# Kernel tuning notes

Measured on AMD Instinct MI355X. Metric: run time of the kernel, lower is better.

Reference implementation:

```python
import jax, jax.numpy as jnp
import numpy as np

N = 131072   # number of profile points
S = 64       # n_samples (PSF samples per point)
D = H = W = 256


def setup_inputs() -> dict:
    key = jax.random.key(0)
    k1, k2, k3, k4, k5, k6 = jax.random.split(key, 6)
    x = jax.random.normal(k1, (1, 1, D, H, W), dtype=jnp.float32)
    # voxel-space coordinates (x, y, z) inside the volume
    sampleGrid = jax.random.uniform(k2, (N, 3), dtype=jnp.float32) * jnp.array(
        [W - 1, H - 1, D - 1], dtype=jnp.float32)
    # small axis-angle rotations + translations: [N, 1, 6]
    rot = jax.random.normal(k3, (N, 1, 3), dtype=jnp.float32) * 0.02
    trn = jax.random.normal(k4, (N, 1, 3), dtype=jnp.float32) * 2.0
    ax = jnp.concatenate([rot, trn], axis=-1)
    half = jax.random.uniform(k5, (N, 1, 3), minval=1.0, maxval=3.0, dtype=jnp.float32)
    bound = jnp.concatenate([-half, half], axis=1)  # [N, 2, 3]
    InvCovScaled = jnp.eye(3, dtype=jnp.float32) * 0.5
    # torch.randn(...) - 0.5 from the original forward, hoisted out for determinism
    xyz_psf = jax.random.normal(k6, (N, S, 3), dtype=jnp.float32) - 0.5
    return dict(x=x, sampleGrid=sampleGrid, ax=ax, bound=bound,
                InvCovScaled=InvCovScaled, xyz_psf=xyz_psf)


def _axisangle2mat(a):
    # a: [N, 6] -> [N, 3, 4] = [R | t] via Rodrigues
    v, t = a[:, :3], a[:, 3:]
    theta = jnp.linalg.norm(v, axis=-1, keepdims=True)          # [N,1]
    k = v / jnp.maximum(theta, 1e-12)                            # unit axis
    kx, ky, kz = k[:, 0], k[:, 1], k[:, 2]
    z = jnp.zeros_like(kx)
    K = jnp.stack([z, -kz, ky, kz, z, -kx, -ky, kx, z], axis=-1).reshape(-1, 3, 3)
    ct = jnp.cos(theta)[..., None]  # [N,1,1]
    st = jnp.sin(theta)[..., None]
    I = jnp.eye(3, dtype=a.dtype)
    R = I + st * K + (1.0 - ct) * jnp.matmul(K, K)
    return jnp.concatenate([R, t[..., None]], axis=-1)           # [N,3,4]


def _grid_sample_3d(vol, grid):
    # vol: [D,H,W]; grid: [M,3] normalized coords (x,y,z) in [-1,1]
    # matches F.grid_sample(mode='bilinear', padding_mode='zeros', align_corners=False)
    d, h, w = vol.shape
    sizes = jnp.array([w, h, d], dtype=vol.dtype)
    pix = ((grid + 1.0) * sizes - 1.0) * 0.5                     # unnormalize
    ix, iy, iz = pix[:, 0], pix[:, 1], pix[:, 2]
    x0 = jnp.floor(ix); y0 = jnp.floor(iy); z0 = jnp.floor(iz)
    fx = ix - x0; fy = iy - y0; fz = iz - z0
    x0 = x0.astype(jnp.int32); y0 = y0.astype(jnp.int32); z0 = z0.astype(jnp.int32)

    def gather(xi, yi, zi):
        valid = ((xi >= 0) & (xi < w) & (yi >= 0) & (yi < h) & (zi >= 0) & (zi < d))
        xc = jnp.clip(xi, 0, w - 1)
        yc = jnp.clip(yi, 0, h - 1)
        zc = jnp.clip(zi, 0, d - 1)
        return jnp.where(valid, vol[zc, yc, xc], jnp.zeros((), vol.dtype))

    out = jnp.zeros(grid.shape[0], dtype=vol.dtype)
    for dx in (0, 1):
        wx = fx if dx else (1.0 - fx)
        for dy in (0, 1):
            wy = fy if dy else (1.0 - fy)
            for dz in (0, 1):
                wz = fz if dz else (1.0 - fz)
                out = out + gather(x0 + dx, y0 + dy, z0 + dz) * (wx * wy * wz)
    return out


def reference(x, sampleGrid, ax, bound, InvCovScaled, xyz_psf):
    vol = x[0, 0]                                                # [D,H,W]
    size = jnp.array([x.shape[-1], x.shape[-2], x.shape[-3]], dtype=x.dtype)  # [W,H,D]

    # pose matrices [N,1,3,4]
    mat = _axisangle2mat(ax.reshape(-1, 6)).reshape(ax.shape[:-1] + (3, 4))
    R = mat[..., :3]                                             # [N,1,3,3]
    T = mat[..., 3]                                              # [N,1,3]
    # trans_first=True: p' = R @ (p + T)
    p = sampleGrid[:, None] + T                                  # [N,1,3]
    mat_sampleGrid = jnp.einsum('nkij,nkj->nki', R, p)           # [N,1,3]

    # PSF offsets: [N,S,3]
    bound_psf = xyz_psf * ((bound[:, 1, :] - bound[:, 0, :]) * 0.5)[:, None]
    psf = mat_sampleGrid + bound_psf                             # [N,S,3]

    grid = 2.0 * (psf / (size - 1.0) - 0.5)                      # normalize per-axis
    psf_x = _grid_sample_3d(vol, grid.reshape(-1, 3)).reshape(psf.shape[:-1])  # [N,S]

    center = bound_psf
    q = jnp.einsum('nsi,ij,nsj->ns', center, InvCovScaled, center)
    w = jnp.exp(-0.5 * q)                                        # [N,S]
    y = (psf_x * w).sum(-1) / w.sum(-1)                          # [N]
    return y
```

## Files before the change

### kernel.cpp

```cpp
#include <hip/hip_runtime.h>


#define VOL_N 256
#define S_PSF 64
#define NBUCKET 4096


__device__ __forceinline__ int bucket_of(const float* __restrict__ sg, int n) {
    int cx = min(max((int)sg[n * 3 + 0], 0), VOL_N - 1) >> 4;
    int cy = min(max((int)sg[n * 3 + 1], 0), VOL_N - 1) >> 4;
    int cz = min(max((int)sg[n * 3 + 2], 0), VOL_N - 1) >> 4;
    int m = 0;
    #pragma unroll
    for (int b = 0; b < 4; b++) {
        m |= (((cx >> b) & 1) << (3 * b))
           | (((cy >> b) & 1) << (3 * b + 1))
           | (((cz >> b) & 1) << (3 * b + 2));
    }
    return m;
}

__global__ void zero_hist_kernel(int* __restrict__ ws) {
    int i = blockIdx.x * blockDim.x + threadIdx.x;
    if (i < NBUCKET) ws[i] = 0;
}

__global__ void hist_kernel(const float* __restrict__ sg, int* __restrict__ ws, int N) {
    int n = blockIdx.x * blockDim.x + threadIdx.x;
    if (n >= N) return;
    atomicAdd(&ws[bucket_of(sg, n)], 1);
}

__global__ __launch_bounds__(1024) void scan_kernel(int* __restrict__ ws) {
    __shared__ int tmp[1024];
    const int t = threadIdx.x;
    int h0 = ws[t * 4 + 0], h1 = ws[t * 4 + 1], h2 = ws[t * 4 + 2], h3 = ws[t * 4 + 3];
    int s = h0 + h1 + h2 + h3;
    tmp[t] = s;
    __syncthreads();
    for (int off = 1; off < 1024; off <<= 1) {
        int v = (t >= off) ? tmp[t - off] : 0;
        __syncthreads();
        tmp[t] += v;
        __syncthreads();
    }
    int excl = tmp[t] - s;
    ws[NBUCKET + t * 4 + 0] = excl;
    ws[NBUCKET + t * 4 + 1] = excl + h0;
    ws[NBUCKET + t * 4 + 2] = excl + h0 + h1;
    ws[NBUCKET + t * 4 + 3] = excl + h0 + h1 + h2;
}

__global__ void scatter_kernel(const float* __restrict__ sg, int* __restrict__ ws, int N) {
    int n = blockIdx.x * blockDim.x + threadIdx.x;
    if (n >= N) return;
    int b = bucket_of(sg, n);
    int pos = atomicAdd(&ws[NBUCKET + b], 1);
    ws[2 * NBUCKET + pos] = n;
}

__global__ __launch_bounds__(256, 4) void psf_sample_kernel(
    const float* __restrict__ vol,
    const float* __restrict__ sampleGrid,
    const float* __restrict__ ax,
    const float* __restrict__ bound,
    const float* __restrict__ invcov,
    const float* __restrict__ xyz_psf,
    const int* __restrict__ perm,
    float* __restrict__ out,
    int N)
{
    const int lane = threadIdx.x & 63;

    int bid = blockIdx.x;
    const int nb = gridDim.x;
    if ((nb & 7) == 0) bid = (bid & 7) * (nb >> 3) + (bid >> 3);

    const int i = bid * (blockDim.x >> 6) + (threadIdx.x >> 6);
    if (i >= N) return;
    const int n = perm ? perm[i] : i;

    const float vx = ax[n * 6 + 0], vy = ax[n * 6 + 1], vz = ax[n * 6 + 2];
    const float tx = ax[n * 6 + 3], ty = ax[n * 6 + 4], tz = ax[n * 6 + 5];

    const float theta = sqrtf(vx * vx + vy * vy + vz * vz);
    const float kinv = 1.0f / fmaxf(theta, 1e-12f);
    const float kx = vx * kinv, ky = vy * kinv, kz = vz * kinv;
    const float ct = __cosf(theta), st = __sinf(theta);
    const float oc = 1.0f - ct;

    const float r00 = 1.0f + oc * (-(ky * ky + kz * kz));
    const float r01 = -st * kz + oc * kx * ky;
    const float r02 =  st * ky + oc * kx * kz;
    const float r10 =  st * kz + oc * kx * ky;
    const float r11 = 1.0f + oc * (-(kx * kx + kz * kz));
    const float r12 = -st * kx + oc * ky * kz;
    const float r20 = -st * ky + oc * kx * kz;
    const float r21 =  st * kx + oc * ky * kz;
    const float r22 = 1.0f + oc * (-(kx * kx + ky * ky));

    const float px = sampleGrid[n * 3 + 0] + tx;
    const float py = sampleGrid[n * 3 + 1] + ty;
    const float pz = sampleGrid[n * 3 + 2] + tz;

    const float cx = r00 * px + r01 * py + r02 * pz;
    const float cy = r10 * px + r11 * py + r12 * pz;
    const float cz = r20 * px + r21 * py + r22 * pz;

    const float hx = (bound[n * 6 + 3] - bound[n * 6 + 0]) * 0.5f;
    const float hy = (bound[n * 6 + 4] - bound[n * 6 + 1]) * 0.5f;
    const float hz = (bound[n * 6 + 5] - bound[n * 6 + 2]) * 0.5f;

    const float m00 = invcov[0], m01 = invcov[1], m02 = invcov[2];
    const float m10 = invcov[3], m11 = invcov[4], m12 = invcov[5];
    const float m20 = invcov[6], m21 = invcov[7], m22 = invcov[8];

    const long long base = ((long long)n * S_PSF + lane) * 3;
    const float ox = xyz_psf[base + 0] * hx;
    const float oy = xyz_psf[base + 1] * hy;
    const float oz = xyz_psf[base + 2] * hz;

    const float scale = (float)VOL_N / (float)(VOL_N - 1);
    const float ix = (cx + ox) * scale - 0.5f;
    const float iy = (cy + oy) * scale - 0.5f;
    const float iz = (cz + oz) * scale - 0.5f;

    const float x0f = floorf(ix), y0f = floorf(iy), z0f = floorf(iz);
    const float fx = ix - x0f, fy = iy - y0f, fz = iz - z0f;
    const int x0 = (int)x0f, y0 = (int)y0f, z0 = (int)z0f;
    const int x1 = x0 + 1, y1 = y0 + 1, z1 = z0 + 1;

    const bool vx0 = (unsigned)x0 < (unsigned)VOL_N;
    const bool vx1 = (unsigned)x1 < (unsigned)VOL_N;
    const bool vy0 = (unsigned)y0 < (unsigned)VOL_N;
    const bool vy1 = (unsigned)y1 < (unsigned)VOL_N;
    const bool vz0 = (unsigned)z0 < (unsigned)VOL_N;
    const bool vz1 = (unsigned)z1 < (unsigned)VOL_N;

    const int xc0 = min(max(x0, 0), VOL_N - 1);
    const int xc1 = min(max(x1, 0), VOL_N - 1);
    const int yc0 = min(max(y0, 0), VOL_N - 1);
    const int yc1 = min(max(y1, 0), VOL_N - 1);
    const int zc0 = min(max(z0, 0), VOL_N - 1);
    const int zc1 = min(max(z1, 0), VOL_N - 1);

    const int zo0 = zc0 * (VOL_N * VOL_N), zo1 = zc1 * (VOL_N * VOL_N);
    const int yo0 = yc0 * VOL_N, yo1 = yc1 * VOL_N;

    const float v000 = vol[zo0 + yo0 + xc0];
    const float v001 = vol[zo0 + yo0 + xc1];
    const float v010 = vol[zo0 + yo1 + xc0];
    const float v011 = vol[zo0 + yo1 + xc1];
    const float v100 = vol[zo1 + yo0 + xc0];
    const float v101 = vol[zo1 + yo0 + xc1];
    const float v110 = vol[zo1 + yo1 + xc0];
    const float v111 = vol[zo1 + yo1 + xc1];

    const float wx0 = 1.0f - fx, wx1 = fx;
    const float wy0 = 1.0f - fy, wy1 = fy;
    const float wz0 = 1.0f - fz, wz1 = fz;

    float acc = 0.0f;
    acc += (vx0 && vy0 && vz0) ? v000 * (wx0 * wy0 * wz0) : 0.0f;
    acc += (vx1 && vy0 && vz0) ? v001 * (wx1 * wy0 * wz0) : 0.0f;
    acc += (vx0 && vy1 && vz0) ? v010 * (wx0 * wy1 * wz0) : 0.0f;
    acc += (vx1 && vy1 && vz0) ? v011 * (wx1 * wy1 * wz0) : 0.0f;
    acc += (vx0 && vy0 && vz1) ? v100 * (wx0 * wy0 * wz1) : 0.0f;
    acc += (vx1 && vy0 && vz1) ? v101 * (wx1 * wy0 * wz1) : 0.0f;
    acc += (vx0 && vy1 && vz1) ? v110 * (wx0 * wy1 * wz1) : 0.0f;
    acc += (vx1 && vy1 && vz1) ? v111 * (wx1 * wy1 * wz1) : 0.0f;

    const float qx = m00 * ox + m01 * oy + m02 * oz;
    const float qy = m10 * ox + m11 * oy + m12 * oz;
    const float qz = m20 * ox + m21 * oy + m22 * oz;
    const float q = ox * qx + oy * qy + oz * qz;
    const float w = __expf(-0.5f * q);

    float num = acc * w;
    float den = w;
    #pragma unroll
    for (int m = 32; m >= 1; m >>= 1) {
        num += __shfl_xor(num, m, 64);
        den += __shfl_xor(den, m, 64);
    }
    if (lane == 0) out[n] = num / den;
}

extern "C" void kernel_launch(void* const* d_in, const int* in_sizes, int n_in,
                              void* d_out, int out_size, void* d_ws, size_t ws_size,
                              hipStream_t stream) {
    const float* x        = (const float*)d_in[0];
    const float* sg       = (const float*)d_in[1];
    const float* ax       = (const float*)d_in[2];
    const float* bound    = (const float*)d_in[3];
    const float* invcov   = (const float*)d_in[4];
    const float* xyz_psf  = (const float*)d_in[5];
    float* out            = (float*)d_out;

    const int N = in_sizes[1] / 3;
    const size_t ws_needed = (size_t)(2 * NBUCKET + N) * sizeof(int);

    int* perm = nullptr;
    if (ws_size >= ws_needed) {
        int* ws = (int*)d_ws;
        zero_hist_kernel<<<(NBUCKET + 255) / 256, 256, 0, stream>>>(ws);
        hist_kernel<<<(N + 255) / 256, 256, 0, stream>>>(sg, ws, N);
        scan_kernel<<<1, 1024, 0, stream>>>(ws);
        scatter_kernel<<<(N + 255) / 256, 256, 0, stream>>>(sg, ws, N);
        perm = ws + 2 * NBUCKET;
    }

    const int waves_per_block = 4;
    dim3 block(256);
    dim3 grid((N + waves_per_block - 1) / waves_per_block);
    psf_sample_kernel<<<grid, block, 0, stream>>>(x, sg, ax, bound, invcov,
                                                  xyz_psf, perm, out, N);
}
```

Measured before the change: 327.9 us.

## Stage per-bucket volume bricks in LDS for trilinear PSF sampling

Buckets points by their rotated center cell instead of the raw grid position, and pads each bucket to a multiple of 16 slots so that each 1024-thread block serves 16 points from a single 16^3 cell. Each block cooperatively loads a 24^3 haloed brick of the volume into shared memory. PSF samples whose 2x2x2 footprint lies inside the brick read it from LDS, and the rest fall back to global gathers. The aim is to replace scattered global gathers with coalesced brick loads plus LDS reads. The cost is a full 55 KB brick load for every block (including sparsely filled padded blocks), many more blocks, and lower occupancy from the large LDS footprint.

After: 454.0 us. 1.38x slower.

```diff
diff --git a/kernel.cpp b/kernel.cpp
--- a/kernel.cpp
+++ b/kernel.cpp
@@ -4,12 +4,50 @@
 #define VOL_N 256
 #define S_PSF 64
 #define NBUCKET 4096
-
-
-__device__ __forceinline__ int bucket_of(const float* __restrict__ sg, int n) {
-    int cx = min(max((int)sg[n * 3 + 0], 0), VOL_N - 1) >> 4;
-    int cy = min(max((int)sg[n * 3 + 1], 0), VOL_N - 1) >> 4;
-    int cz = min(max((int)sg[n * 3 + 2], 0), VOL_N - 1) >> 4;
+#define HALO 4
+#define BRICK 24
+#define BRICK_YSTR 25
+#define BRICK_ZSTR 600
+#define BRICK_VOX (BRICK * BRICK * BRICK)
+#define LDS_FLOATS (BRICK * BRICK_ZSTR)
+#define SPB 16
+
+
+__device__ __forceinline__ void sample_center(const float* __restrict__ sg,
+                                              const float* __restrict__ ax,
+                                              int n, float& cx, float& cy, float& cz) {
+    const float vx = ax[n * 6 + 0], vy = ax[n * 6 + 1], vz = ax[n * 6 + 2];
+    const float tx = ax[n * 6 + 3], ty = ax[n * 6 + 4], tz = ax[n * 6 + 5];
+    const float theta = sqrtf(vx * vx + vy * vy + vz * vz);
+    const float kinv = 1.0f / fmaxf(theta, 1e-12f);
+    const float kx = vx * kinv, ky = vy * kinv, kz = vz * kinv;
+    const float ct = __cosf(theta), st = __sinf(theta);
+    const float oc = 1.0f - ct;
+    const float r00 = 1.0f + oc * (-(ky * ky + kz * kz));
+    const float r01 = -st * kz + oc * kx * ky;
+    const float r02 =  st * ky + oc * kx * kz;
+    const float r10 =  st * kz + oc * kx * ky;
+    const float r11 = 1.0f + oc * (-(kx * kx + kz * kz));
+    const float r12 = -st * kx + oc * ky * kz;
+    const float r20 = -st * ky + oc * kx * kz;
+    const float r21 =  st * kx + oc * ky * kz;
+    const float r22 = 1.0f + oc * (-(kx * kx + ky * ky));
+    const float px = sg[n * 3 + 0] + tx;
+    const float py = sg[n * 3 + 1] + ty;
+    const float pz = sg[n * 3 + 2] + tz;
+    cx = r00 * px + r01 * py + r02 * pz;
+    cy = r10 * px + r11 * py + r12 * pz;
+    cz = r20 * px + r21 * py + r22 * pz;
+}
+
+__device__ __forceinline__ void cell_of_center(float cx, float cy, float cz,
+                                               int& ix, int& iy, int& iz) {
+    ix = min(max((int)cx, 0), VOL_N - 1) >> 4;
+    iy = min(max((int)cy, 0), VOL_N - 1) >> 4;
+    iz = min(max((int)cz, 0), VOL_N - 1) >> 4;
+}
+
+__device__ __forceinline__ int morton3(int cx, int cy, int cz) {
     int m = 0;
     #pragma unroll
     for (int b = 0; b < 4; b++) {
@@ -25,17 +63,30 @@
     if (i < NBUCKET) ws[i] = 0;
 }
 
-__global__ void hist_kernel(const float* __restrict__ sg, int* __restrict__ ws, int N) {
+__global__ void fill_perm_kernel(int* __restrict__ ws, int nslot) {
+    int i = blockIdx.x * blockDim.x + threadIdx.x;
+    if (i < nslot) ws[2 * NBUCKET + i] = -1;
+}
+
+__global__ void hist_kernel(const float* __restrict__ sg, const float* __restrict__ ax,
+                            int* __restrict__ ws, int N) {
     int n = blockIdx.x * blockDim.x + threadIdx.x;
     if (n >= N) return;
-    atomicAdd(&ws[bucket_of(sg, n)], 1);
+    float cx, cy, cz;
+    sample_center(sg, ax, n, cx, cy, cz);
+    int ix, iy, iz;
+    cell_of_center(cx, cy, cz, ix, iy, iz);
+    atomicAdd(&ws[morton3(ix, iy, iz)], 1);
 }
 
 __global__ __launch_bounds__(1024) void scan_kernel(int* __restrict__ ws) {
     __shared__ int tmp[1024];
     const int t = threadIdx.x;
-    int h0 = ws[t * 4 + 0], h1 = ws[t * 4 + 1], h2 = ws[t * 4 + 2], h3 = ws[t * 4 + 3];
-    int s = h0 + h1 + h2 + h3;
+    int p0 = (ws[t * 4 + 0] + SPB - 1) & ~(SPB - 1);
+    int p1 = (ws[t * 4 + 1] + SPB - 1) & ~(SPB - 1);
+    int p2 = (ws[t * 4 + 2] + SPB - 1) & ~(SPB - 1);
+    int p3 = (ws[t * 4 + 3] + SPB - 1) & ~(SPB - 1);
+    int s = p0 + p1 + p2 + p3;
     tmp[t] = s;
     __syncthreads();
     for (int off = 1; off < 1024; off <<= 1) {
@@ -46,20 +97,25 @@
     }
     int excl = tmp[t] - s;
     ws[NBUCKET + t * 4 + 0] = excl;
-    ws[NBUCKET + t * 4 + 1] = excl + h0;
-    ws[NBUCKET + t * 4 + 2] = excl + h0 + h1;
-    ws[NBUCKET + t * 4 + 3] = excl + h0 + h1 + h2;
-}
-
-__global__ void scatter_kernel(const float* __restrict__ sg, int* __restrict__ ws, int N) {
+    ws[NBUCKET + t * 4 + 1] = excl + p0;
+    ws[NBUCKET + t * 4 + 2] = excl + p0 + p1;
+    ws[NBUCKET + t * 4 + 3] = excl + p0 + p1 + p2;
+}
+
+__global__ void scatter_kernel(const float* __restrict__ sg, const float* __restrict__ ax,
+                               int* __restrict__ ws, int N) {
     int n = blockIdx.x * blockDim.x + threadIdx.x;
     if (n >= N) return;
-    int b = bucket_of(sg, n);
+    float cx, cy, cz;
+    sample_center(sg, ax, n, cx, cy, cz);
+    int ix, iy, iz;
+    cell_of_center(cx, cy, cz, ix, iy, iz);
+    int b = morton3(ix, iy, iz);
     int pos = atomicAdd(&ws[NBUCKET + b], 1);
     ws[2 * NBUCKET + pos] = n;
 }
 
-__global__ __launch_bounds__(256, 4) void psf_sample_kernel(
+__global__ __launch_bounds__(1024, 8) void psf_sample_kernel(
     const float* __restrict__ vol,
     const float* __restrict__ sampleGrid,
     const float* __restrict__ ax,
@@ -70,25 +126,52 @@
     float* __restrict__ out,
     int N)
 {
-    const int lane = threadIdx.x & 63;
+    __shared__ float lds[LDS_FLOATS];
+
+    const int tid = threadIdx.x;
+    const int lane = tid & 63;
+    const int wave = tid >> 6;
 
     int bid = blockIdx.x;
     const int nb = gridDim.x;
     if ((nb & 7) == 0) bid = (bid & 7) * (nb >> 3) + (bid >> 3);
 
-    const int i = bid * (blockDim.x >> 6) + (threadIdx.x >> 6);
-    if (i >= N) return;
-    const int n = perm ? perm[i] : i;
+    const int slot_base = bid * SPB;
+    const int n0 = perm ? perm[slot_base] : (slot_base < N ? slot_base : -1);
+    if (n0 < 0) return;
+
+    float ccx, ccy, ccz;
+    sample_center(sampleGrid, ax, n0, ccx, ccy, ccz);
+    int cix, ciy, ciz;
+    cell_of_center(ccx, ccy, ccz, cix, ciy, ciz);
+    const int bx0 = (cix << 4) - HALO;
+    const int by0 = (ciy << 4) - HALO;
+    const int bz0 = (ciz << 4) - HALO;
+
+    for (int t = tid; t < BRICK_VOX; t += 1024) {
+        const int z = t / (BRICK * BRICK);
+        const int r = t - z * (BRICK * BRICK);
+        const int y = r / BRICK;
+        const int x = r - y * BRICK;
+        const int gx = bx0 + x, gy = by0 + y, gz = bz0 + z;
+        float v = 0.0f;
+        if ((unsigned)gx < VOL_N && (unsigned)gy < VOL_N && (unsigned)gz < VOL_N)
+            v = vol[(gz << 16) + (gy << 8) + gx];
+        lds[z * BRICK_ZSTR + y * BRICK_YSTR + x] = v;
+    }
+    __syncthreads();
+
+    const int slot = slot_base + wave;
+    const int n = perm ? perm[slot] : (slot < N ? slot : -1);
+    if (n < 0) return;
 
     const float vx = ax[n * 6 + 0], vy = ax[n * 6 + 1], vz = ax[n * 6 + 2];
     const float tx = ax[n * 6 + 3], ty = ax[n * 6 + 4], tz = ax[n * 6 + 5];
-
     const float theta = sqrtf(vx * vx + vy * vy + vz * vz);
     const float kinv = 1.0f / fmaxf(theta, 1e-12f);
     const float kx = vx * kinv, ky = vy * kinv, kz = vz * kinv;
     const float ct = __cosf(theta), st = __sinf(theta);
     const float oc = 1.0f - ct;
-
     const float r00 = 1.0f + oc * (-(ky * ky + kz * kz));
     const float r01 = -st * kz + oc * kx * ky;
     const float r02 =  st * ky + oc * kx * kz;
@@ -98,11 +181,9 @@
     const float r20 = -st * ky + oc * kx * kz;
     const float r21 =  st * kx + oc * ky * kz;
     const float r22 = 1.0f + oc * (-(kx * kx + ky * ky));
-
     const float px = sampleGrid[n * 3 + 0] + tx;
     const float py = sampleGrid[n * 3 + 1] + ty;
     const float pz = sampleGrid[n * 3 + 2] + tz;
-
     const float cx = r00 * px + r01 * py + r02 * pz;
     const float cy = r10 * px + r11 * py + r12 * pz;
     const float cz = r20 * px + r21 * py + r22 * pz;
@@ -115,10 +196,10 @@
     const float m10 = invcov[3], m11 = invcov[4], m12 = invcov[5];
     const float m20 = invcov[6], m21 = invcov[7], m22 = invcov[8];
 
-    const long long base = ((long long)n * S_PSF + lane) * 3;
-    const float ox = xyz_psf[base + 0] * hx;
-    const float oy = xyz_psf[base + 1] * hy;
-    const float oz = xyz_psf[base + 2] * hz;
+    const long long pbase = ((long long)n * S_PSF + lane) * 3;
+    const float ox = xyz_psf[pbase + 0] * hx;
+    const float oy = xyz_psf[pbase + 1] * hy;
+    const float oz = xyz_psf[pbase + 2] * hz;
 
     const float scale = (float)VOL_N / (float)(VOL_N - 1);
     const float ix = (cx + ox) * scale - 0.5f;
@@ -128,47 +209,58 @@
     const float x0f = floorf(ix), y0f = floorf(iy), z0f = floorf(iz);
     const float fx = ix - x0f, fy = iy - y0f, fz = iz - z0f;
     const int x0 = (int)x0f, y0 = (int)y0f, z0 = (int)z0f;
-    const int x1 = x0 + 1, y1 = y0 + 1, z1 = z0 + 1;
-
-    const bool vx0 = (unsigned)x0 < (unsigned)VOL_N;
-    const bool vx1 = (unsigned)x1 < (unsigned)VOL_N;
-    const bool vy0 = (unsigned)y0 < (unsigned)VOL_N;
-    const bool vy1 = (unsigned)y1 < (unsigned)VOL_N;
-    const bool vz0 = (unsigned)z0 < (unsigned)VOL_N;
-    const bool vz1 = (unsigned)z1 < (unsigned)VOL_N;
-
-    const int xc0 = min(max(x0, 0), VOL_N - 1);
-    const int xc1 = min(max(x1, 0), VOL_N - 1);
-    const int yc0 = min(max(y0, 0), VOL_N - 1);
-    const int yc1 = min(max(y1, 0), VOL_N - 1);
-    const int zc0 = min(max(z0, 0), VOL_N - 1);
-    const int zc1 = min(max(z1, 0), VOL_N - 1);
-
-    const int zo0 = zc0 * (VOL_N * VOL_N), zo1 = zc1 * (VOL_N * VOL_N);
-    const int yo0 = yc0 * VOL_N, yo1 = yc1 * VOL_N;
-
-    const float v000 = vol[zo0 + yo0 + xc0];
-    const float v001 = vol[zo0 + yo0 + xc1];
-    const float v010 = vol[zo0 + yo1 + xc0];
-    const float v011 = vol[zo0 + yo1 + xc1];
-    const float v100 = vol[zo1 + yo0 + xc0];
-    const float v101 = vol[zo1 + yo0 + xc1];
-    const float v110 = vol[zo1 + yo1 + xc0];
-    const float v111 = vol[zo1 + yo1 + xc1];
 
     const float wx0 = 1.0f - fx, wx1 = fx;
     const float wy0 = 1.0f - fy, wy1 = fy;
     const float wz0 = 1.0f - fz, wz1 = fz;
 
-    float acc = 0.0f;
-    acc += (vx0 && vy0 && vz0) ? v000 * (wx0 * wy0 * wz0) : 0.0f;
-    acc += (vx1 && vy0 && vz0) ? v001 * (wx1 * wy0 * wz0) : 0.0f;
-    acc += (vx0 && vy1 && vz0) ? v010 * (wx0 * wy1 * wz0) : 0.0f;
-    acc += (vx1 && vy1 && vz0) ? v011 * (wx1 * wy1 * wz0) : 0.0f;
-    acc += (vx0 && vy0 && vz1) ? v100 * (wx0 * wy0 * wz1) : 0.0f;
-    acc += (vx1 && vy0 && vz1) ? v101 * (wx1 * wy0 * wz1) : 0.0f;
-    acc += (vx0 && vy1 && vz1) ? v110 * (wx0 * wy1 * wz1) : 0.0f;
-    acc += (vx1 && vy1 && vz1) ? v111 * (wx1 * wy1 * wz1) : 0.0f;
+    const int rx = x0 - bx0, ry = y0 - by0, rz = z0 - bz0;
+    const bool fast = (unsigned)rx <= (BRICK - 2) && (unsigned)ry <= (BRICK - 2)
+                   && (unsigned)rz <= (BRICK - 2);
+
+    float acc;
+    if (fast) {
+        const int a = rz * BRICK_ZSTR + ry * BRICK_YSTR + rx;
+        const float v000 = lds[a];
+        const float v001 = lds[a + 1];
+        const float v010 = lds[a + BRICK_YSTR];
+        const float v011 = lds[a + BRICK_YSTR + 1];
+        const float v100 = lds[a + BRICK_ZSTR];
+        const float v101 = lds[a + BRICK_ZSTR + 1];
+        const float v110 = lds[a + BRICK_ZSTR + BRICK_YSTR];
+        const float v111 = lds[a + BRICK_ZSTR + BRICK_YSTR + 1];
+        acc = v000 * (wx0 * wy0 * wz0) + v001 * (wx1 * wy0 * wz0)
+            + v010 * (wx0 * wy1 * wz0) + v011 * (wx1 * wy1 * wz0)
+            + v100 * (wx0 * wy0 * wz1) + v101 * (wx1 * wy0 * wz1)
+            + v110 * (wx0 * wy1 * wz1) + v111 * (wx1 * wy1 * wz1);
+    } else {
+        const int x1 = x0 + 1, y1 = y0 + 1, z1 = z0 + 1;
+        const bool vx0 = (unsigned)x0 < VOL_N, vx1 = (unsigned)x1 < VOL_N;
+        const bool vy0 = (unsigned)y0 < VOL_N, vy1 = (unsigned)y1 < VOL_N;
+        const bool vz0 = (unsigned)z0 < VOL_N, vz1 = (unsigned)z1 < VOL_N;
+        const int xc0 = min(max(x0, 0), VOL_N - 1), xc1 = min(max(x1, 0), VOL_N - 1);
+        const int yc0 = min(max(y0, 0), VOL_N - 1), yc1 = min(max(y1, 0), VOL_N - 1);
+        const int zc0 = min(max(z0, 0), VOL_N - 1), zc1 = min(max(z1, 0), VOL_N - 1);
+        const int zo0 = zc0 << 16, zo1 = zc1 << 16;
+        const int yo0 = yc0 << 8, yo1 = yc1 << 8;
+        const float v000 = vol[zo0 + yo0 + xc0];
+        const float v001 = vol[zo0 + yo0 + xc1];
+        const float v010 = vol[zo0 + yo1 + xc0];
+        const float v011 = vol[zo0 + yo1 + xc1];
+        const float v100 = vol[zo1 + yo0 + xc0];
+        const float v101 = vol[zo1 + yo0 + xc1];
+        const float v110 = vol[zo1 + yo1 + xc0];
+        const float v111 = vol[zo1 + yo1 + xc1];
+        acc = 0.0f;
+        acc += (vx0 && vy0 && vz0) ? v000 * (wx0 * wy0 * wz0) : 0.0f;
+        acc += (vx1 && vy0 && vz0) ? v001 * (wx1 * wy0 * wz0) : 0.0f;
+        acc += (vx0 && vy1 && vz0) ? v010 * (wx0 * wy1 * wz0) : 0.0f;
+        acc += (vx1 && vy1 && vz0) ? v011 * (wx1 * wy1 * wz0) : 0.0f;
+        acc += (vx0 && vy0 && vz1) ? v100 * (wx0 * wy0 * wz1) : 0.0f;
+        acc += (vx1 && vy0 && vz1) ? v101 * (wx1 * wy0 * wz1) : 0.0f;
+        acc += (vx0 && vy1 && vz1) ? v110 * (wx0 * wy1 * wz1) : 0.0f;
+        acc += (vx1 && vy1 && vz1) ? v111 * (wx1 * wy1 * wz1) : 0.0f;
+    }
 
     const float qx = m00 * ox + m01 * oy + m02 * oz;
     const float qy = m10 * ox + m11 * oy + m12 * oz;
@@ -198,21 +290,24 @@
     float* out            = (float*)d_out;
 
     const int N = in_sizes[1] / 3;
-    const size_t ws_needed = (size_t)(2 * NBUCKET + N) * sizeof(int);
+    const int nslot = N + SPB * NBUCKET;
+    const size_t ws_needed = (size_t)(2 * NBUCKET + nslot) * sizeof(int);
 
     int* perm = nullptr;
+    int nblocks;
     if (ws_size >= ws_needed) {
         int* ws = (int*)d_ws;
         zero_hist_kernel<<<(NBUCKET + 255) / 256, 256, 0, stream>>>(ws);
-        hist_kernel<<<(N + 255) / 256, 256, 0, stream>>>(sg, ws, N);
+        fill_perm_kernel<<<(nslot + 1023) / 1024, 1024, 0, stream>>>(ws, nslot);
+        hist_kernel<<<(N + 255) / 256, 256, 0, stream>>>(sg, ax, ws, N);
         scan_kernel<<<1, 1024, 0, stream>>>(ws);
-        scatter_kernel<<<(N + 255) / 256, 256, 0, stream>>>(sg, ws, N);
+        scatter_kernel<<<(N + 255) / 256, 256, 0, stream>>>(sg, ax, ws, N);
         perm = ws + 2 * NBUCKET;
-    }
-
-    const int waves_per_block = 4;
-    dim3 block(256);
-    dim3 grid((N + waves_per_block - 1) / waves_per_block);
-    psf_sample_kernel<<<grid, block, 0, stream>>>(x, sg, ax, bound, invcov,
-                                                  xyz_psf, perm, out, N);
-}
+        nblocks = nslot / SPB;
+    } else {
+        nblocks = (N + SPB - 1) / SPB;
+    }
+
+    psf_sample_kernel<<<nblocks, 1024, 0, stream>>>(x, sg, ax, bound, invcov,
+                                                    xyz_psf, perm, out, N);
+}
```

## Build x-neighbor paired volume so trilinear gathers use four float2 loads

Applied to the files above, without the earlier changes.

Adds a pre-pass that writes each voxel together with its +x neighbor into a 128MB interleaved pairs buffer in workspace. The sampling kernel then fetches four float2 values instead of eight scalar floats per trilinear sample, selecting the right element at the clamped x boundary. This halves the number of gather instructions but costs a full read of the 64MB volume and a 128MB write on every call, and it doubles the footprint that the random gathers touch. It only takes effect when the workspace is large enough, otherwise it falls back to the old path.

Measured after the change: 375.8 us. +14.6%, slower.

```diff
diff --git a/kernel.cpp b/kernel.cpp
--- a/kernel.cpp
+++ b/kernel.cpp
@@ -4,6 +4,10 @@
 #define VOL_N 256
 #define S_PSF 64
 #define NBUCKET 4096
+#define PAIRS_ELEMS (1 << 24)
+#define PAIRS_BYTES ((size_t)PAIRS_ELEMS * 8)
+
+typedef float vf4 __attribute__((ext_vector_type(4)));
 
 
 __device__ __forceinline__ int bucket_of(const float* __restrict__ sg, int n) {
@@ -59,8 +63,24 @@
     ws[2 * NBUCKET + pos] = n;
 }
 
+__global__ __launch_bounds__(256) void build_pairs_kernel(
+    const float* __restrict__ vol, float* __restrict__ pairs) {
+    const int g4 = blockIdx.x * blockDim.x + threadIdx.x;
+    const int g = g4 << 2;
+    const vf4 v = *(const vf4*)(vol + g);
+    const int x = g & (VOL_N - 1);
+    const float nxt = (x == VOL_N - 4) ? v.w : __builtin_nontemporal_load(vol + g + 4);
+    vf4* dst = (vf4*)(pairs + (size_t)g * 2);
+    vf4 a; a.x = v.x; a.y = v.y; a.z = v.y; a.w = v.z;
+    vf4 b; b.x = v.z; b.y = v.w; b.z = v.w; b.w = nxt;
+    __builtin_nontemporal_store(a, dst);
+    __builtin_nontemporal_store(b, dst + 1);
+}
+
+template <bool USE_PAIRS>
 __global__ __launch_bounds__(256, 4) void psf_sample_kernel(
     const float* __restrict__ vol,
+    const float2* __restrict__ pairs,
     const float* __restrict__ sampleGrid,
     const float* __restrict__ ax,
     const float* __restrict__ bound,
@@ -137,24 +157,38 @@
     const bool vz0 = (unsigned)z0 < (unsigned)VOL_N;
     const bool vz1 = (unsigned)z1 < (unsigned)VOL_N;
 
-    const int xc0 = min(max(x0, 0), VOL_N - 1);
-    const int xc1 = min(max(x1, 0), VOL_N - 1);
     const int yc0 = min(max(y0, 0), VOL_N - 1);
     const int yc1 = min(max(y1, 0), VOL_N - 1);
     const int zc0 = min(max(z0, 0), VOL_N - 1);
     const int zc1 = min(max(z1, 0), VOL_N - 1);
-
-    const int zo0 = zc0 * (VOL_N * VOL_N), zo1 = zc1 * (VOL_N * VOL_N);
-    const int yo0 = yc0 * VOL_N, yo1 = yc1 * VOL_N;
-
-    const float v000 = vol[zo0 + yo0 + xc0];
-    const float v001 = vol[zo0 + yo0 + xc1];
-    const float v010 = vol[zo0 + yo1 + xc0];
-    const float v011 = vol[zo0 + yo1 + xc1];
-    const float v100 = vol[zo1 + yo0 + xc0];
-    const float v101 = vol[zo1 + yo0 + xc1];
-    const float v110 = vol[zo1 + yo1 + xc0];
-    const float v111 = vol[zo1 + yo1 + xc1];
+    const int zo0 = zc0 << 16, zo1 = zc1 << 16;
+    const int yo0 = yc0 << 8, yo1 = yc1 << 8;
+
+    float v000, v001, v010, v011, v100, v101, v110, v111;
+    if (USE_PAIRS) {
+        const int xg = min(max(x0, 0), VOL_N - 2);
+        const int dx = x0 - xg;
+        const bool hi = (dx == 1), lo = (dx == -1);
+        const float2 p00 = pairs[zo0 + yo0 + xg];
+        const float2 p01 = pairs[zo0 + yo1 + xg];
+        const float2 p10 = pairs[zo1 + yo0 + xg];
+        const float2 p11 = pairs[zo1 + yo1 + xg];
+        v000 = hi ? p00.y : p00.x;  v001 = lo ? p00.x : p00.y;
+        v010 = hi ? p01.y : p01.x;  v011 = lo ? p01.x : p01.y;
+        v100 = hi ? p10.y : p10.x;  v101 = lo ? p10.x : p10.y;
+        v110 = hi ? p11.y : p11.x;  v111 = lo ? p11.x : p11.y;
+    } else {
+        const int xc0 = min(max(x0, 0), VOL_N - 1);
+        const int xc1 = min(max(x1, 0), VOL_N - 1);
+        v000 = vol[zo0 + yo0 + xc0];
+        v001 = vol[zo0 + yo0 + xc1];
+        v010 = vol[zo0 + yo1 + xc0];
+        v011 = vol[zo0 + yo1 + xc1];
+        v100 = vol[zo1 + yo0 + xc0];
+        v101 = vol[zo1 + yo0 + xc1];
+        v110 = vol[zo1 + yo1 + xc0];
+        v111 = vol[zo1 + yo1 + xc1];
+    }
 
     const float wx0 = 1.0f - fx, wx1 = fx;
     const float wy0 = 1.0f - fy, wy1 = fy;
@@ -198,21 +232,33 @@
     float* out            = (float*)d_out;
 
     const int N = in_sizes[1] / 3;
-    const size_t ws_needed = (size_t)(2 * NBUCKET + N) * sizeof(int);
+    const size_t sort_bytes = (size_t)(2 * NBUCKET + N) * sizeof(int);
+
+    const bool use_pairs = ws_size >= PAIRS_BYTES + sort_bytes;
+    const bool use_sort  = use_pairs || ws_size >= sort_bytes;
+
+    float* pairs = use_pairs ? (float*)d_ws : nullptr;
+    int* sort_ws = use_pairs ? (int*)((char*)d_ws + PAIRS_BYTES) : (int*)d_ws;
 
     int* perm = nullptr;
-    if (ws_size >= ws_needed) {
-        int* ws = (int*)d_ws;
-        zero_hist_kernel<<<(NBUCKET + 255) / 256, 256, 0, stream>>>(ws);
-        hist_kernel<<<(N + 255) / 256, 256, 0, stream>>>(sg, ws, N);
-        scan_kernel<<<1, 1024, 0, stream>>>(ws);
-        scatter_kernel<<<(N + 255) / 256, 256, 0, stream>>>(sg, ws, N);
-        perm = ws + 2 * NBUCKET;
-    }
-
-    const int waves_per_block = 4;
+    if (use_sort) {
+        zero_hist_kernel<<<(NBUCKET + 255) / 256, 256, 0, stream>>>(sort_ws);
+        hist_kernel<<<(N + 255) / 256, 256, 0, stream>>>(sg, sort_ws, N);
+        scan_kernel<<<1, 1024, 0, stream>>>(sort_ws);
+        scatter_kernel<<<(N + 255) / 256, 256, 0, stream>>>(sg, sort_ws, N);
+        perm = sort_ws + 2 * NBUCKET;
+    }
+    if (use_pairs) {
+        build_pairs_kernel<<<(PAIRS_ELEMS / 4) / 256, 256, 0, stream>>>(x, pairs);
+    }
+
     dim3 block(256);
-    dim3 grid((N + waves_per_block - 1) / waves_per_block);
-    psf_sample_kernel<<<grid, block, 0, stream>>>(x, sg, ax, bound, invcov,
-                                                  xyz_psf, perm, out, N);
-}
+    dim3 grid((N + 3) / 4);
+    if (use_pairs) {
+        psf_sample_kernel<true><<<grid, block, 0, stream>>>(
+            x, (const float2*)pairs, sg, ax, bound, invcov, xyz_psf, perm, out, N);
+    } else {
+        psf_sample_kernel<false><<<grid, block, 0, stream>>>(
+            x, nullptr, sg, ax, bound, invcov, xyz_psf, perm, out, N);
+    }
+}
```
